# Optimization experiments

Measured on AMD Instinct MI355X. Metric: run time of the kernel, lower is better.

Reference implementation:

```python
import jax, jax.numpy as jnp
import numpy as np

B, T, C, H = 4, 2048, 1024, 16
D = C // H  # head_dim = 64

def setup_inputs() -> dict:
    key = jax.random.key(0)
    k1, k2, k3 = jax.random.split(key, 3)
    x = jax.random.normal(k1, (B, T, C), dtype=jnp.float32)
    W_attn = jax.random.normal(k2, (C, 3 * C), dtype=jnp.float32) * (C ** -0.5)
    b_attn = jnp.zeros((3 * C,), dtype=jnp.float32)
    W_proj = jax.random.normal(k3, (C, C), dtype=jnp.float32) * (C ** -0.5)
    b_proj = jnp.zeros((C,), dtype=jnp.float32)
    return {"x": x, "W_attn": W_attn, "b_attn": b_attn, "W_proj": W_proj, "b_proj": b_proj}

def reference(x, W_attn, b_attn, W_proj, b_proj):
    Bc, Tc, Cc = x.shape
    qkv = x @ W_attn + b_attn                       # [B,T,3C]
    q, k, v = jnp.split(qkv, 3, axis=-1)
    q = q.reshape(Bc, Tc, H, D).transpose(0, 2, 1, 3)  # [B,H,T,D]
    k = k.reshape(Bc, Tc, H, D).transpose(0, 2, 1, 3)
    v = v.reshape(Bc, Tc, H, D).transpose(0, 2, 1, 3)
    scores = jnp.einsum('bhqd,bhkd->bhqk', q, k) / jnp.sqrt(jnp.float32(D))
    causal = jnp.tril(jnp.ones((Tc, Tc), dtype=bool))
    scores = jnp.where(causal[None, None, :, :], scores, jnp.float32(-jnp.inf))
    wei = jax.nn.softmax(scores, axis=-1)           # dropout=0 -> identity
    out = jnp.einsum('bhqk,bhkd->bhqd', wei, v)     # [B,H,T,D]
    out = out.transpose(0, 2, 1, 3).reshape(Bc, Tc, Cc)
    return out @ W_proj + b_proj
```

## Files before the change

kernel.cpp:

```cpp
#include <hip/hip_runtime.h>
#include <cstdint>
#include <cstddef>

#define Bsz   4
#define Tsz   2048
#define Csz   1024
#define Hn    16
#define Dh    64
#define Mrows 8192
#define KD    1024

#define NEG_BIG (-1.0e30f)
#define SCL2  0.18033688011112042f

typedef unsigned short u16;
typedef __bf16  bf16x8 __attribute__((ext_vector_type(8)));
typedef __bf16  bf16x2 __attribute__((ext_vector_type(2)));
typedef float   f32x4  __attribute__((ext_vector_type(4)));
typedef unsigned int u32x4 __attribute__((ext_vector_type(4)));

#define BARRIER() do { asm volatile("" ::: "memory");                          \
                       __builtin_amdgcn_s_barrier();                           \
                       asm volatile("" ::: "memory"); } while (0)

__device__ __forceinline__ u16 f2bf(float f) {
  union { float f; unsigned int i; } v; v.f = f;
  unsigned int u = v.i;
  return (u16)((u + 0x7fffu + ((u >> 16) & 1u)) >> 16);
}
__device__ __forceinline__ unsigned int pack2bf(float a, float b) {
#if __has_builtin(__builtin_amdgcn_cvt_pk_bf16_f32)
  union { bf16x2 h; unsigned int u; } cv;
  cv.h = __builtin_amdgcn_cvt_pk_bf16_f32(a, b);
  return cv.u;
#else
  return (unsigned int)f2bf(a) | ((unsigned int)f2bf(b) << 16);
#endif
}
__device__ __forceinline__ unsigned int pack2bf_trunc(float lo, float hi) {
  return __builtin_amdgcn_perm(__builtin_bit_cast(unsigned int, hi),
                               __builtin_bit_cast(unsigned int, lo),
                               0x07060302u);
}
__device__ __forceinline__ float fast_exp2(float x) {
#if __has_builtin(__builtin_amdgcn_exp2f)
  return __builtin_amdgcn_exp2f(x);
#else
  return exp2f(x);
#endif
}

#define CVT_BLKS  (Mrows * Csz / 4 / 256)
#define TRA_BLKS  (48 * 16)
#define TRP_BLKS  (16 * 16)

__global__ __launch_bounds__(256)
void prep(const float* __restrict__ x, u16* __restrict__ xbf,
          const float* __restrict__ Wa, u16* __restrict__ WTa,
          const float* __restrict__ Wp, u16* __restrict__ WTp) {
  __shared__ u16 tile[64][65];
  int bid = blockIdx.x;
  const int tid = threadIdx.x;
  if (bid < CVT_BLKS) {
    const int i = bid * 256 + tid;
    const float4 v = ((const float4*)x)[i];
    uint2 o;
    o.x = pack2bf(v.x, v.y);
    o.y = pack2bf(v.z, v.w);
    ((uint2*)xbf)[i] = o;
    return;
  }
  bid -= CVT_BLKS;
  const float* in; u16* out; int cols, bx, by;
  if (bid < TRA_BLKS) {
    in = Wa; out = WTa; cols = 3 * Csz; bx = bid % 48; by = bid / 48;
  } else {
    bid -= TRA_BLKS;
    in = Wp; out = WTp; cols = Csz; bx = bid & 15; by = bid >> 4;
  }
  const int tc = bx * 64, tr = by * 64;
  const int xx = tid & 63, y0 = tid >> 6;
#pragma unroll
  for (int yy = 0; yy < 64; yy += 4) {
    int r = yy + y0;
    tile[r][xx] = f2bf(in[(size_t)(tr + r) * cols + tc + xx]);
  }
  __syncthreads();
#pragma unroll
  for (int yy = 0; yy < 64; yy += 4) {
    int r = yy + y0;
    out[(size_t)(tc + r) * Csz + tr + xx] = tile[xx][r];
  }
}

template<int MODE>
__global__ __launch_bounds__(256, 4)
void gemm_bt(const u16* __restrict__ A, const u16* __restrict__ BT,
             const float* __restrict__ bias, u16* __restrict__ o0,
             u16* __restrict__ o1, u16* __restrict__ o2,
             float* __restrict__ fout, int N) {
  __shared__ u16 lsA[2][128 * 32];
  __shared__ u16 lsB[2][128 * 32];
  const int tid  = threadIdx.x;
  const int lane = tid & 63;
  const int wid  = tid >> 6;
  const int wm   = wid & 1, wn = wid >> 1;
  const int quad = lane >> 4, l15 = lane & 15;
  const int rswz = (l15 >> 1) & 3;

  int bx, by;
  {
    const int nwg  = gridDim.x * gridDim.y;
    const int orig = (int)blockIdx.y * gridDim.x + (int)blockIdx.x;
    const int cpx  = nwg >> 3;
    const int swz  = (orig & 7) * cpx + (orig >> 3);
    bx = swz % gridDim.x; by = swz / gridDim.x;
  }
  const int m0 = by * 128, n0 = bx * 128;

  f32x4 acc[4][4];
#pragma unroll
  for (int i = 0; i < 4; ++i)
#pragma unroll
    for (int j = 0; j < 4; ++j) acc[i][j] = (f32x4){0.f, 0.f, 0.f, 0.f};

  const int srow   = lane >> 2;
  const int schunk = (lane & 3) ^ ((lane >> 3) & 3);
  const u16* gA = A  + (size_t)(m0 + wid * 32 + srow) * KD + schunk * 8;
  const u16* gB = BT + (size_t)(n0 + wid * 32 + srow) * KD + schunk * 8;

  auto gstage = [&](int t, int bb) {
#if __has_builtin(__builtin_amdgcn_global_load_lds)
#pragma unroll
    for (int i = 0; i < 2; ++i)
      __builtin_amdgcn_global_load_lds(
          (const __attribute__((address_space(1))) void*)(gA + (size_t)i * 16 * KD + t * 32),
          (__attribute__((address_space(3))) void*)(&lsA[bb][(wid * 32 + i * 16) * 32]),
          16, 0, 0);
#pragma unroll
    for (int i = 0; i < 2; ++i)
      __builtin_amdgcn_global_load_lds(
          (const __attribute__((address_space(1))) void*)(gB + (size_t)i * 16 * KD + t * 32),
          (__attribute__((address_space(3))) void*)(&lsB[bb][(wid * 32 + i * 16) * 32]),
          16, 0, 0);
#else
#pragma unroll
    for (int cc = 0; cc < 2; ++cc) {
      const int c = tid + cc * 256;
      const int rr = c >> 2, off = c & 3;
      const int dc = (off ^ ((rr >> 1) & 3)) << 3;
      *(uint4*)&lsA[bb][rr * 32 + dc] =
          *(const uint4*)&A[(size_t)(m0 + rr) * KD + t * 32 + off * 8];
    }
#pragma unroll
    for (int cc = 0; cc < 2; ++cc) {
      const int c = tid + cc * 256;
      const int rr = c >> 2, off = c & 3;
      const int dc = (off ^ ((rr >> 1) & 3)) << 3;
      *(uint4*)&lsB[bb][rr * 32 + dc] =
          *(const uint4*)&BT[(size_t)(n0 + rr) * KD + t * 32 + off * 8];
    }
#endif
  };

#define READ_B(n_) (*(const bf16x8*)                                           \
    &lsB[cur][(wn * 64 + (n_) * 16 + l15) * 32 + ((quad ^ rswz) << 3)])
#define READ_A(m_) (*(const bf16x8*)                                           \
    &lsA[cur][(wm * 64 + (m_) * 16 + l15) * 32 + ((quad ^ rswz) << 3)])
#define MFMA_ROW(m_, src)                                                      \
  __builtin_amdgcn_s_setprio(1);                                               \
  _Pragma("unroll")                                                            \
  for (int n = 0; n < 4; ++n)                                                  \
    acc[m_][n] = __builtin_amdgcn_mfma_f32_16x16x32_bf16(                      \
        src, bfv[n], acc[m_][n], 0, 0, 0);                                     \
  __builtin_amdgcn_s_setprio(0);

  gstage(0, 0);
  const int KT = KD / 32;
  for (int t = 0; t < KT; ++t) {
    const int cur = t & 1;
    if (t < KT - 1) {
      gstage(t + 1, cur ^ 1);
      asm volatile("s_waitcnt vmcnt(4)" ::: "memory");
    } else {
      asm volatile("s_waitcnt vmcnt(0)" ::: "memory");
    }
    BARRIER();

    bf16x8 bfv[4];
#pragma unroll
    for (int n = 0; n < 4; ++n) bfv[n] = READ_B(n);
    bf16x8 afA = READ_A(0);
    bf16x8 afB = READ_A(1);
    MFMA_ROW(0, afA);
    afA = READ_A(2);
    MFMA_ROW(1, afB);
    afB = READ_A(3);
    MFMA_ROW(2, afA);
    MFMA_ROW(3, afB);

    BARRIER();
  }
#undef READ_B
#undef READ_A
#undef MFMA_ROW

#pragma unroll
  for (int i = 0; i < 4; ++i) {
#pragma unroll
    for (int j = 0; j < 4; ++j) {
      const int colb = n0 + wn * 64 + j * 16 + l15;
      const float bv = bias[colb];
      float vals[4];
#pragma unroll
      for (int r = 0; r < 4; ++r) vals[r] = acc[i][j][r] + bv;
      const int row0 = m0 + wm * 64 + i * 16 + quad * 4;
      if (MODE == 0) {
        const int b = row0 >> 11, t0 = row0 & (Tsz - 1);
        const int region = colb >> 10;
        const int nc = colb & (Csz - 1);
        const int h = nc >> 6, d = nc & 63;
        if (region == 2) {
          uint2 st;
          st.x = pack2bf(vals[0], vals[1]);
          st.y = pack2bf(vals[2], vals[3]);
          *(uint2*)&o2[((size_t)((b << 4) + h) * Dh + d) * Tsz + t0] = st;
        } else {
          u16* dst = (region == 0) ? o0 : o1;
          const float qs = (region == 0) ? SCL2 : 1.0f;
#pragma unroll
          for (int r = 0; r < 4; ++r)
            dst[(size_t)(((b << 4) + h) * Tsz + t0 + r) * Dh + d] =
                f2bf(vals[r] * qs);
        }
      } else {
#pragma unroll
        for (int r = 0; r < 4; ++r)
          fout[(size_t)(row0 + r) * N + colb] = vals[r];
      }
    }
  }
}

__global__ __launch_bounds__(256)
void attn_fused(const u16* __restrict__ qb, const u16* __restrict__ kbuf,
                const u16* __restrict__ vT, u16* __restrict__ outp) {
  __shared__ u16 Kl[2][64 * 64];
  __shared__ u16 Vt[2][64 * 64];
  const int tid = threadIdx.x, lane = tid & 63, w = tid >> 6;
  const int quad = lane >> 4, l15 = lane & 15;
  const int cswz = (l15 & 7) << 3;
  const int bh = blockIdx.x;
  const int b = bh >> 4, h = bh & 15;
  const u16* Q   = qb   + (size_t)bh * Tsz * Dh;
  const u16* Kg  = kbuf + (size_t)bh * Tsz * Dh;
  const u16* VTg = vT   + (size_t)bh * Dh * Tsz;

  const int srow   = lane >> 3;
  const int schunk = ((lane & 7) ^ srow) << 3;
  const u16* gK0 = Kg  + (size_t)(w * 16 + srow) * Dh  + schunk;
  const u16* gV0 = VTg + (size_t)(w * 16 + srow) * Tsz + schunk;

#if __has_builtin(__builtin_amdgcn_global_load_lds)
#define STAGE(jj, bb) do {                                                     \
    const size_t kb_ = (size_t)(jj) * 64;                                      \
    _Pragma("unroll")                                                          \
    for (int i_ = 0; i_ < 2; ++i_) {                                           \
      __builtin_amdgcn_global_load_lds(                                        \
        (const __attribute__((address_space(1))) void*)(gK0 + (kb_ + (size_t)i_ * 8) * Dh), \
        (__attribute__((address_space(3))) void*)(&Kl[bb][(w * 16 + i_ * 8) * 64]), 16, 0, 0); \
      __builtin_amdgcn_global_load_lds(                                        \
        (const __attribute__((address_space(1))) void*)(gV0 + (size_t)(i_ * 8) * Tsz + kb_), \
        (__attribute__((address_space(3))) void*)(&Vt[bb][(w * 16 + i_ * 8) * 64]), 16, 0, 0); \
    }                                                                          \
  } while (0)
#else
#define STAGE(jj, bb) do {                                                     \
    const int kb_ = (jj) * 64;                                                 \
    _Pragma("unroll")                                                          \
    for (int cc_ = 0; cc_ < 2; ++cc_) {                                        \
      const int c_ = tid + cc_ * 256;                                          \
      const int rr_ = c_ >> 3, off_ = c_ & 7;                                  \
      const int dc_ = (off_ ^ (rr_ & 7)) << 3;                                 \
      *(uint4*)&Kl[bb][rr_ * 64 + dc_] =                                       \
          *(const uint4*)&Kg[(size_t)(kb_ + rr_) * Dh + off_ * 8];             \
      *(uint4*)&Vt[bb][rr_ * 64 + dc_] =                                       \
          *(const uint4*)&VTg[(size_t)rr_ * Tsz + kb_ + off_ * 8];             \
    }                                                                          \
  } while (0)
#endif

  for (int ph = 0; ph < 2; ++ph) {
    const int jq = ph ? (int)blockIdx.y : 31 - (int)blockIdx.y;

    const int qrow = jq * 64 + w * 16 + l15;
    const bf16x8 bq0 = *(const bf16x8*)&Q[(size_t)qrow * Dh + quad * 8];
    const bf16x8 bq1 = *(const bf16x8*)&Q[(size_t)qrow * Dh + 32 + quad * 8];

    f32x4 O[4];
#pragma unroll
    for (int nb = 0; nb < 4; ++nb) O[nb] = (f32x4){0.f, 0.f, 0.f, 0.f};
    float l_i = 0.f;

    STAGE(0, 0);

    for (int j = 0; j <= jq; ++j) {
      const int cur = j & 1;
      if (j < jq) {
        STAGE(j + 1, cur ^ 1);
        asm volatile("s_waitcnt vmcnt(4)" ::: "memory");
      } else {
        asm volatile("s_waitcnt vmcnt(0)" ::: "memory");
      }
      BARRIER();

      const int kb = j * 64;
      const bool diag = (j == jq);
      const int tmax = diag ? (w + 1) : 4;
      const u16* KT = Kl[cur];
      const u16* VL = Vt[cur];

      f32x4 S[4];
#pragma unroll
      for (int t = 0; t < 4; ++t) S[t] = (f32x4){0.f, 0.f, 0.f, 0.f};
      __builtin_amdgcn_s_setprio(1);
#pragma unroll
      for (int t = 0; t < 4; ++t) {
        if (t < tmax) {
          bf16x8 ak = *(const bf16x8*)&KT[(t * 16 + l15) * 64 + ((quad * 8) ^ cswz)];
          S[t] = __builtin_amdgcn_mfma_f32_16x16x32_bf16(ak, bq0, S[t], 0, 0, 0);
          ak = *(const bf16x8*)&KT[(t * 16 + l15) * 64 + ((quad * 8 + 32) ^ cswz)];
          S[t] = __builtin_amdgcn_mfma_f32_16x16x32_bf16(ak, bq1, S[t], 0, 0, 0);
        }
      }
      __builtin_amdgcn_s_setprio(0);

      float p[4][4];
      if (diag) {
#pragma unroll
        for (int t = 0; t < 4; ++t) {
          const int key0 = kb + t * 16 + quad * 4;
#pragma unroll
          for (int r = 0; r < 4; ++r) {
            const float sv =
                (t < tmax && key0 + r <= qrow) ? S[t][r] : NEG_BIG;
            p[t][r] = fast_exp2(sv);
            l_i += p[t][r];
          }
        }
      } else {
#pragma unroll
        for (int t = 0; t < 4; ++t)
#pragma unroll
          for (int r = 0; r < 4; ++r) {
            p[t][r] = fast_exp2(S[t][r]);
            l_i += p[t][r];
          }
      }

      u32x4 pu;
      pu[0] = pack2bf_trunc(p[0][0], p[0][1]);
      pu[1] = pack2bf_trunc(p[0][2], p[0][3]);
      pu[2] = pack2bf_trunc(p[1][0], p[1][1]);
      pu[3] = pack2bf_trunc(p[1][2], p[1][3]);
      bf16x8 pb = __builtin_bit_cast(bf16x8, pu);
      __builtin_amdgcn_s_setprio(1);
#pragma unroll
      for (int nb = 0; nb < 4; ++nb) {
        const uint2 a0 = *(const uint2*)&VL[(nb * 16 + l15) * 64 + ((quad * 4) ^ cswz)];
        const uint2 a1 = *(const uint2*)&VL[(nb * 16 + l15) * 64 + ((quad * 4 + 16) ^ cswz)];
        const u32x4 au = {a0.x, a0.y, a1.x, a1.y};
        O[nb] = __builtin_amdgcn_mfma_f32_16x16x32_bf16(
            __builtin_bit_cast(bf16x8, au), pb, O[nb], 0, 0, 0);
      }
      __builtin_amdgcn_s_setprio(0);
      if (tmax > 2) {
        pu[0] = pack2bf_trunc(p[2][0], p[2][1]);
        pu[1] = pack2bf_trunc(p[2][2], p[2][3]);
        pu[2] = pack2bf_trunc(p[3][0], p[3][1]);
        pu[3] = pack2bf_trunc(p[3][2], p[3][3]);
        pb = __builtin_bit_cast(bf16x8, pu);
        __builtin_amdgcn_s_setprio(1);
#pragma unroll
        for (int nb = 0; nb < 4; ++nb) {
          const uint2 a0 = *(const uint2*)&VL[(nb * 16 + l15) * 64 + ((quad * 4 + 32) ^ cswz)];
          const uint2 a1 = *(const uint2*)&VL[(nb * 16 + l15) * 64 + ((quad * 4 + 48) ^ cswz)];
          const u32x4 au = {a0.x, a0.y, a1.x, a1.y};
          O[nb] = __builtin_amdgcn_mfma_f32_16x16x32_bf16(
              __builtin_bit_cast(bf16x8, au), pb, O[nb], 0, 0, 0);
        }
        __builtin_amdgcn_s_setprio(0);
      }
      BARRIER();
    }

    float lt = l_i + __shfl_xor(l_i, 16, 64);
    lt += __shfl_xor(lt, 32, 64);
    const float inv = 1.0f / lt;
#pragma unroll
    for (int nb = 0; nb < 4; ++nb) {
      uint2 st;
      st.x = pack2bf(O[nb][0] * inv, O[nb][1] * inv);
      st.y = pack2bf(O[nb][2] * inv, O[nb][3] * inv);
      *(uint2*)&outp[(size_t)(b * Tsz + qrow) * Csz + h * Dh + nb * 16 + quad * 4] = st;
    }
  }
#undef STAGE
}

extern "C" void kernel_launch(void* const* d_in, const int* in_sizes, int n_in,
                              void* d_out, int out_size, void* d_ws, size_t ws_size,
                              hipStream_t stream) {
  const float* x      = (const float*)d_in[0];
  const float* W_attn = (const float*)d_in[1];
  const float* b_attn = (const float*)d_in[2];
  const float* W_proj = (const float*)d_in[3];
  const float* b_proj = (const float*)d_in[4];
  float* out = (float*)d_out;

  u16* ws   = (u16*)d_ws;
  u16* xbf  = ws;
  u16* qbuf = xbf  + (size_t)Mrows * Csz;
  u16* kbuf = qbuf + (size_t)Mrows * Csz;
  u16* vbuf = kbuf + (size_t)Mrows * Csz;
  u16* aout = vbuf + (size_t)Mrows * Csz;
  u16* WTa  = aout + (size_t)Mrows * Csz;
  u16* WTp  = WTa  + (size_t)Csz * 3 * Csz;

  prep<<<CVT_BLKS + TRA_BLKS + TRP_BLKS, 256, 0, stream>>>(
      x, xbf, W_attn, WTa, W_proj, WTp);
  gemm_bt<0><<<dim3(3 * Csz / 128, Mrows / 128), dim3(256), 0, stream>>>(
      xbf, WTa, b_attn, qbuf, kbuf, vbuf, nullptr, 3 * Csz);
  attn_fused<<<dim3(Bsz * Hn, Tsz / 128), 256, 0, stream>>>(
      qbuf, kbuf, vbuf, aout);
  gemm_bt<1><<<dim3(Csz / 128, Mrows / 128), dim3(256), 0, stream>>>(
      aout, WTp, b_proj, nullptr, nullptr, nullptr, out, Csz);
}
```

Baseline: 244.0 us.

## Templatize GEMM tiles, use 256-wide blocks with 4-stage LDS pipeline

The bf16 GEMM kernel is templated on block and warp tile sizes, and both projection GEMMs now launch 512-thread blocks with larger tiles (256x256 for QKV, 256x128 for output). The LDS ring grows from double to quad buffering, prefetching three k-steps ahead with matching vmcnt waits. The aim is more operand reuse per global load and deeper latency hiding. The cost is much more LDS and register use per block, fewer blocks, and possibly worse wave quantization on 256 CUs.

```diff
diff --git a/kernel.cpp b/kernel.cpp
--- a/kernel.cpp
+++ b/kernel.cpp
@@ -22,6 +22,16 @@
 #define BARRIER() do { asm volatile("" ::: "memory");                          \
                        __builtin_amdgcn_s_barrier();                           \
                        asm volatile("" ::: "memory"); } while (0)
+
+template<int N> __device__ __forceinline__ void vmwait() {
+  if constexpr (N >= 12)     asm volatile("s_waitcnt vmcnt(12)" ::: "memory");
+  else if constexpr (N == 9) asm volatile("s_waitcnt vmcnt(9)"  ::: "memory");
+  else if constexpr (N == 8) asm volatile("s_waitcnt vmcnt(8)"  ::: "memory");
+  else if constexpr (N == 6) asm volatile("s_waitcnt vmcnt(6)"  ::: "memory");
+  else if constexpr (N == 4) asm volatile("s_waitcnt vmcnt(4)"  ::: "memory");
+  else if constexpr (N == 3) asm volatile("s_waitcnt vmcnt(3)"  ::: "memory");
+  else                       asm volatile("s_waitcnt vmcnt(0)"  ::: "memory");
+}
 
 __device__ __forceinline__ u16 f2bf(float f) {
   union { float f; unsigned int i; } v; v.f = f;
@@ -93,18 +103,26 @@
   }
 }
 
-template<int MODE>
-__global__ __launch_bounds__(256, 4)
+template<int BM, int BN, int WM, int WN, int MODE>
+__global__ __launch_bounds__((BM / WM) * (BN / WN) * 64, 2)
 void gemm_bt(const u16* __restrict__ A, const u16* __restrict__ BT,
              const float* __restrict__ bias, u16* __restrict__ o0,
              u16* __restrict__ o1, u16* __restrict__ o2,
              float* __restrict__ fout, int N) {
-  __shared__ u16 lsA[2][128 * 32];
-  __shared__ u16 lsB[2][128 * 32];
+  constexpr int NW   = (BM / WM) * (BN / WN);
+  constexpr int WNV  = BN / WN;
+  constexpr int MF_M = WM / 16;
+  constexpr int MF_N = WN / 16;
+  constexpr int AI   = (BM / NW) / 16;
+  constexpr int BI   = (BN / NW) / 16;
+  constexpr int PI   = AI + BI;
+
+  __shared__ u16 lsA[4][BM * 32];
+  __shared__ u16 lsB[4][BN * 32];
   const int tid  = threadIdx.x;
   const int lane = tid & 63;
   const int wid  = tid >> 6;
-  const int wm   = wid & 1, wn = wid >> 1;
+  const int wm   = wid / WNV, wn = wid % WNV;
   const int quad = lane >> 4, l15 = lane & 15;
   const int rswz = (l15 >> 1) & 3;
 
@@ -116,45 +134,45 @@
     const int swz  = (orig & 7) * cpx + (orig >> 3);
     bx = swz % gridDim.x; by = swz / gridDim.x;
   }
-  const int m0 = by * 128, n0 = bx * 128;
-
-  f32x4 acc[4][4];
-#pragma unroll
-  for (int i = 0; i < 4; ++i)
-#pragma unroll
-    for (int j = 0; j < 4; ++j) acc[i][j] = (f32x4){0.f, 0.f, 0.f, 0.f};
+  const int m0 = by * BM, n0 = bx * BN;
+
+  f32x4 acc[MF_M][MF_N];
+#pragma unroll
+  for (int i = 0; i < MF_M; ++i)
+#pragma unroll
+    for (int j = 0; j < MF_N; ++j) acc[i][j] = (f32x4){0.f, 0.f, 0.f, 0.f};
 
   const int srow   = lane >> 2;
   const int schunk = (lane & 3) ^ ((lane >> 3) & 3);
-  const u16* gA = A  + (size_t)(m0 + wid * 32 + srow) * KD + schunk * 8;
-  const u16* gB = BT + (size_t)(n0 + wid * 32 + srow) * KD + schunk * 8;
+  const u16* gA = A  + (size_t)(m0 + wid * (BM / NW) + srow) * KD + schunk * 8;
+  const u16* gB = BT + (size_t)(n0 + wid * (BN / NW) + srow) * KD + schunk * 8;
 
   auto gstage = [&](int t, int bb) {
 #if __has_builtin(__builtin_amdgcn_global_load_lds)
 #pragma unroll
-    for (int i = 0; i < 2; ++i)
+    for (int i = 0; i < AI; ++i)
       __builtin_amdgcn_global_load_lds(
           (const __attribute__((address_space(1))) void*)(gA + (size_t)i * 16 * KD + t * 32),
-          (__attribute__((address_space(3))) void*)(&lsA[bb][(wid * 32 + i * 16) * 32]),
+          (__attribute__((address_space(3))) void*)(&lsA[bb][(wid * (BM / NW) + i * 16) * 32]),
           16, 0, 0);
 #pragma unroll
-    for (int i = 0; i < 2; ++i)
+    for (int i = 0; i < BI; ++i)
       __builtin_amdgcn_global_load_lds(
           (const __attribute__((address_space(1))) void*)(gB + (size_t)i * 16 * KD + t * 32),
-          (__attribute__((address_space(3))) void*)(&lsB[bb][(wid * 32 + i * 16) * 32]),
+          (__attribute__((address_space(3))) void*)(&lsB[bb][(wid * (BN / NW) + i * 16) * 32]),
           16, 0, 0);
 #else
 #pragma unroll
-    for (int cc = 0; cc < 2; ++cc) {
-      const int c = tid + cc * 256;
+    for (int cc = 0; cc < BM * 4 / (NW * 64); ++cc) {
+      const int c = tid + cc * NW * 64;
       const int rr = c >> 2, off = c & 3;
       const int dc = (off ^ ((rr >> 1) & 3)) << 3;
       *(uint4*)&lsA[bb][rr * 32 + dc] =
           *(const uint4*)&A[(size_t)(m0 + rr) * KD + t * 32 + off * 8];
     }
 #pragma unroll
-    for (int cc = 0; cc < 2; ++cc) {
-      const int c = tid + cc * 256;
+    for (int cc = 0; cc < BN * 4 / (NW * 64); ++cc) {
+      const int c = tid + cc * NW * 64;
       const int rr = c >> 2, off = c & 3;
       const int dc = (off ^ ((rr >> 1) & 3)) << 3;
       *(uint4*)&lsB[bb][rr * 32 + dc] =
@@ -164,57 +182,56 @@
   };
 
 #define READ_B(n_) (*(const bf16x8*)                                           \
-    &lsB[cur][(wn * 64 + (n_) * 16 + l15) * 32 + ((quad ^ rswz) << 3)])
+    &lsB[cur][(wn * WN + (n_) * 16 + l15) * 32 + ((quad ^ rswz) << 3)])
 #define READ_A(m_) (*(const bf16x8*)                                           \
-    &lsA[cur][(wm * 64 + (m_) * 16 + l15) * 32 + ((quad ^ rswz) << 3)])
-#define MFMA_ROW(m_, src)                                                      \
-  __builtin_amdgcn_s_setprio(1);                                               \
-  _Pragma("unroll")                                                            \
-  for (int n = 0; n < 4; ++n)                                                  \
-    acc[m_][n] = __builtin_amdgcn_mfma_f32_16x16x32_bf16(                      \
-        src, bfv[n], acc[m_][n], 0, 0, 0);                                     \
-  __builtin_amdgcn_s_setprio(0);
-
-  gstage(0, 0);
+    &lsA[cur][(wm * WM + (m_) * 16 + l15) * 32 + ((quad ^ rswz) << 3)])
+
+  gstage(0, 0); gstage(1, 1); gstage(2, 2);
   const int KT = KD / 32;
   for (int t = 0; t < KT; ++t) {
-    const int cur = t & 1;
-    if (t < KT - 1) {
-      gstage(t + 1, cur ^ 1);
-      asm volatile("s_waitcnt vmcnt(4)" ::: "memory");
-    } else {
-      asm volatile("s_waitcnt vmcnt(0)" ::: "memory");
-    }
+    const int cur = t & 3;
+    if (t + 3 < KT) {
+      gstage(t + 3, (t + 3) & 3);
+      vmwait<3 * PI>();
+    } else if (t == KT - 3) vmwait<2 * PI>();
+    else if (t == KT - 2)   vmwait<PI>();
+    else                    vmwait<0>();
     BARRIER();
 
-    bf16x8 bfv[4];
-#pragma unroll
-    for (int n = 0; n < 4; ++n) bfv[n] = READ_B(n);
-    bf16x8 afA = READ_A(0);
-    bf16x8 afB = READ_A(1);
-    MFMA_ROW(0, afA);
-    afA = READ_A(2);
-    MFMA_ROW(1, afB);
-    afB = READ_A(3);
-    MFMA_ROW(2, afA);
-    MFMA_ROW(3, afB);
+    bf16x8 bfv[MF_N];
+#pragma unroll
+    for (int n = 0; n < MF_N; ++n) bfv[n] = READ_B(n);
+    bf16x8 ar0 = READ_A(0);
+    bf16x8 ar1 = READ_A(1);
+#pragma unroll
+    for (int m = 0; m < MF_M; ++m) {
+      const bf16x8 am = (m & 1) ? ar1 : ar0;
+      if (m + 2 < MF_M) {
+        if (m & 1) ar1 = READ_A(m + 2); else ar0 = READ_A(m + 2);
+      }
+      __builtin_amdgcn_s_setprio(1);
+#pragma unroll
+      for (int n = 0; n < MF_N; ++n)
+        acc[m][n] = __builtin_amdgcn_mfma_f32_16x16x32_bf16(
+            am, bfv[n], acc[m][n], 0, 0, 0);
+      __builtin_amdgcn_s_setprio(0);
+    }
 
     BARRIER();
   }
 #undef READ_B
 #undef READ_A
-#undef MFMA_ROW
-
-#pragma unroll
-  for (int i = 0; i < 4; ++i) {
-#pragma unroll
-    for (int j = 0; j < 4; ++j) {
-      const int colb = n0 + wn * 64 + j * 16 + l15;
+
+#pragma unroll
+  for (int i = 0; i < MF_M; ++i) {
+#pragma unroll
+    for (int j = 0; j < MF_N; ++j) {
+      const int colb = n0 + wn * WN + j * 16 + l15;
       const float bv = bias[colb];
       float vals[4];
 #pragma unroll
       for (int r = 0; r < 4; ++r) vals[r] = acc[i][j][r] + bv;
-      const int row0 = m0 + wm * 64 + i * 16 + quad * 4;
+      const int row0 = m0 + wm * WM + i * 16 + quad * 4;
       if (MODE == 0) {
         const int b = row0 >> 11, t0 = row0 & (Tsz - 1);
         const int region = colb >> 10;
@@ -429,10 +446,12 @@
 
   prep<<<CVT_BLKS + TRA_BLKS + TRP_BLKS, 256, 0, stream>>>(
       x, xbf, W_attn, WTa, W_proj, WTp);
-  gemm_bt<0><<<dim3(3 * Csz / 128, Mrows / 128), dim3(256), 0, stream>>>(
+  gemm_bt<256, 256, 128, 64, 0><<<dim3(3 * Csz / 256, Mrows / 256),
+                                  dim3(512), 0, stream>>>(
       xbf, WTa, b_attn, qbuf, kbuf, vbuf, nullptr, 3 * Csz);
   attn_fused<<<dim3(Bsz * Hn, Tsz / 128), 256, 0, stream>>>(
       qbuf, kbuf, vbuf, aout);
-  gemm_bt<1><<<dim3(Csz / 128, Mrows / 128), dim3(256), 0, stream>>>(
+  gemm_bt<256, 128, 64, 64, 1><<<dim3(Csz / 128, Mrows / 256),
+                                 dim3(512), 0, stream>>>(
       aout, WTp, b_proj, nullptr, nullptr, nullptr, out, Csz);
 }
```

New measurement: 269.6 us. 1.1x slower.

## Template GEMM tile sizes with wider QKV tile; compute softmax row sums via MFMA

Applied to the files above, without the earlier changes.

The GEMM kernel becomes a template over block tile dimensions. The QKV projection now runs with 128x256 tiles and 8 waves per block, which gives more B-operand reuse per A load and cuts the grid to half as many blocks. In the attention kernel, the per-lane scalar accumulation of softmax probabilities and the closing cross-lane shuffle reduction are replaced by an extra MFMA against a ones vector, so the row sums come out of the matrix unit. The extra MFMA per step adds matrix-core work, and the larger GEMM block increases LDS and register pressure, which may lower occupancy.

```diff
diff --git a/kernel.cpp b/kernel.cpp
--- a/kernel.cpp
+++ b/kernel.cpp
@@ -22,6 +22,14 @@
 #define BARRIER() do { asm volatile("" ::: "memory");                          \
                        __builtin_amdgcn_s_barrier();                           \
                        asm volatile("" ::: "memory"); } while (0)
+
+template<int N> __device__ __forceinline__ void vmwait() {
+  if constexpr (N >= 8)      asm volatile("s_waitcnt vmcnt(8)"  ::: "memory");
+  else if constexpr (N == 6) asm volatile("s_waitcnt vmcnt(6)"  ::: "memory");
+  else if constexpr (N == 4) asm volatile("s_waitcnt vmcnt(4)"  ::: "memory");
+  else if constexpr (N == 3) asm volatile("s_waitcnt vmcnt(3)"  ::: "memory");
+  else                       asm volatile("s_waitcnt vmcnt(0)"  ::: "memory");
+}
 
 __device__ __forceinline__ u16 f2bf(float f) {
   union { float f; unsigned int i; } v; v.f = f;
@@ -93,18 +101,24 @@
   }
 }
 
-template<int MODE>
-__global__ __launch_bounds__(256, 4)
+template<int BM, int BN, int MODE>
+__global__ __launch_bounds__((BM / 64) * (BN / 64) * 64, 4)
 void gemm_bt(const u16* __restrict__ A, const u16* __restrict__ BT,
              const float* __restrict__ bias, u16* __restrict__ o0,
              u16* __restrict__ o1, u16* __restrict__ o2,
              float* __restrict__ fout, int N) {
-  __shared__ u16 lsA[2][128 * 32];
-  __shared__ u16 lsB[2][128 * 32];
+  constexpr int NW  = (BM / 64) * (BN / 64);
+  constexpr int WNV = BN / 64;
+  constexpr int AI  = (BM / NW) / 16;
+  constexpr int BI  = (BN / NW) / 16;
+  constexpr int PI  = AI + BI;
+
+  __shared__ u16 lsA[2][BM * 32];
+  __shared__ u16 lsB[2][BN * 32];
   const int tid  = threadIdx.x;
   const int lane = tid & 63;
   const int wid  = tid >> 6;
-  const int wm   = wid & 1, wn = wid >> 1;
+  const int wm   = wid / WNV, wn = wid % WNV;
   const int quad = lane >> 4, l15 = lane & 15;
   const int rswz = (l15 >> 1) & 3;
 
@@ -116,7 +130,7 @@
     const int swz  = (orig & 7) * cpx + (orig >> 3);
     bx = swz % gridDim.x; by = swz / gridDim.x;
   }
-  const int m0 = by * 128, n0 = bx * 128;
+  const int m0 = by * BM, n0 = bx * BN;
 
   f32x4 acc[4][4];
 #pragma unroll
@@ -126,35 +140,35 @@
 
   const int srow   = lane >> 2;
   const int schunk = (lane & 3) ^ ((lane >> 3) & 3);
-  const u16* gA = A  + (size_t)(m0 + wid * 32 + srow) * KD + schunk * 8;
-  const u16* gB = BT + (size_t)(n0 + wid * 32 + srow) * KD + schunk * 8;
+  const u16* gA = A  + (size_t)(m0 + wid * (BM / NW) + srow) * KD + schunk * 8;
+  const u16* gB = BT + (size_t)(n0 + wid * (BN / NW) + srow) * KD + schunk * 8;
 
   auto gstage = [&](int t, int bb) {
 #if __has_builtin(__builtin_amdgcn_global_load_lds)
 #pragma unroll
-    for (int i = 0; i < 2; ++i)
+    for (int i = 0; i < AI; ++i)
       __builtin_amdgcn_global_load_lds(
           (const __attribute__((address_space(1))) void*)(gA + (size_t)i * 16 * KD + t * 32),
-          (__attribute__((address_space(3))) void*)(&lsA[bb][(wid * 32 + i * 16) * 32]),
+          (__attribute__((address_space(3))) void*)(&lsA[bb][(wid * (BM / NW) + i * 16) * 32]),
           16, 0, 0);
 #pragma unroll
-    for (int i = 0; i < 2; ++i)
+    for (int i = 0; i < BI; ++i)
       __builtin_amdgcn_global_load_lds(
           (const __attribute__((address_space(1))) void*)(gB + (size_t)i * 16 * KD + t * 32),
-          (__attribute__((address_space(3))) void*)(&lsB[bb][(wid * 32 + i * 16) * 32]),
+          (__attribute__((address_space(3))) void*)(&lsB[bb][(wid * (BN / NW) + i * 16) * 32]),
           16, 0, 0);
 #else
 #pragma unroll
-    for (int cc = 0; cc < 2; ++cc) {
-      const int c = tid + cc * 256;
+    for (int cc = 0; cc < BM * 4 / (NW * 64); ++cc) {
+      const int c = tid + cc * NW * 64;
       const int rr = c >> 2, off = c & 3;
       const int dc = (off ^ ((rr >> 1) & 3)) << 3;
       *(uint4*)&lsA[bb][rr * 32 + dc] =
           *(const uint4*)&A[(size_t)(m0 + rr) * KD + t * 32 + off * 8];
     }
 #pragma unroll
-    for (int cc = 0; cc < 2; ++cc) {
-      const int c = tid + cc * 256;
+    for (int cc = 0; cc < BN * 4 / (NW * 64); ++cc) {
+      const int c = tid + cc * NW * 64;
       const int rr = c >> 2, off = c & 3;
       const int dc = (off ^ ((rr >> 1) & 3)) << 3;
       *(uint4*)&lsB[bb][rr * 32 + dc] =
@@ -181,9 +195,9 @@
     const int cur = t & 1;
     if (t < KT - 1) {
       gstage(t + 1, cur ^ 1);
-      asm volatile("s_waitcnt vmcnt(4)" ::: "memory");
+      vmwait<PI>();
     } else {
-      asm volatile("s_waitcnt vmcnt(0)" ::: "memory");
+      vmwait<0>();
     }
     BARRIER();
 
@@ -255,6 +269,9 @@
   const u16* Q   = qb   + (size_t)bh * Tsz * Dh;
   const u16* Kg  = kbuf + (size_t)bh * Tsz * Dh;
   const u16* VTg = vT   + (size_t)bh * Dh * Tsz;
+
+  const u32x4 onesu = {0x3F803F80u, 0x3F803F80u, 0x3F803F80u, 0x3F803F80u};
+  const bf16x8 ones = __builtin_bit_cast(bf16x8, onesu);
 
   const int srow   = lane >> 3;
   const int schunk = ((lane & 7) ^ srow) << 3;
@@ -300,7 +317,7 @@
     f32x4 O[4];
 #pragma unroll
     for (int nb = 0; nb < 4; ++nb) O[nb] = (f32x4){0.f, 0.f, 0.f, 0.f};
-    float l_i = 0.f;
+    f32x4 lmf = (f32x4){0.f, 0.f, 0.f, 0.f};
 
     STAGE(0, 0);
 
@@ -345,17 +362,14 @@
             const float sv =
                 (t < tmax && key0 + r <= qrow) ? S[t][r] : NEG_BIG;
             p[t][r] = fast_exp2(sv);
-            l_i += p[t][r];
           }
         }
       } else {
 #pragma unroll
         for (int t = 0; t < 4; ++t)
 #pragma unroll
-          for (int r = 0; r < 4; ++r) {
+          for (int r = 0; r < 4; ++r)
             p[t][r] = fast_exp2(S[t][r]);
-            l_i += p[t][r];
-          }
       }
 
       u32x4 pu;
@@ -373,6 +387,7 @@
         O[nb] = __builtin_amdgcn_mfma_f32_16x16x32_bf16(
             __builtin_bit_cast(bf16x8, au), pb, O[nb], 0, 0, 0);
       }
+      lmf = __builtin_amdgcn_mfma_f32_16x16x32_bf16(ones, pb, lmf, 0, 0, 0);
       __builtin_amdgcn_s_setprio(0);
       if (tmax > 2) {
         pu[0] = pack2bf_trunc(p[2][0], p[2][1]);
@@ -389,14 +404,13 @@
           O[nb] = __builtin_amdgcn_mfma_f32_16x16x32_bf16(
               __builtin_bit_cast(bf16x8, au), pb, O[nb], 0, 0, 0);
         }
+        lmf = __builtin_amdgcn_mfma_f32_16x16x32_bf16(ones, pb, lmf, 0, 0, 0);
         __builtin_amdgcn_s_setprio(0);
       }
       BARRIER();
     }
 
-    float lt = l_i + __shfl_xor(l_i, 16, 64);
-    lt += __shfl_xor(lt, 32, 64);
-    const float inv = 1.0f / lt;
+    const float inv = 1.0f / lmf[0];
 #pragma unroll
     for (int nb = 0; nb < 4; ++nb) {
       uint2 st;
@@ -429,10 +443,10 @@
 
   prep<<<CVT_BLKS + TRA_BLKS + TRP_BLKS, 256, 0, stream>>>(
       x, xbf, W_attn, WTa, W_proj, WTp);
-  gemm_bt<0><<<dim3(3 * Csz / 128, Mrows / 128), dim3(256), 0, stream>>>(
+  gemm_bt<128, 256, 0><<<dim3(3 * Csz / 256, Mrows / 128), dim3(512), 0, stream>>>(
       xbf, WTa, b_attn, qbuf, kbuf, vbuf, nullptr, 3 * Csz);
   attn_fused<<<dim3(Bsz * Hn, Tsz / 128), 256, 0, stream>>>(
       qbuf, kbuf, vbuf, aout);
-  gemm_bt<1><<<dim3(Csz / 128, Mrows / 128), dim3(256), 0, stream>>>(
+  gemm_bt<128, 128, 1><<<dim3(Csz / 128, Mrows / 128), dim3(256), 0, stream>>>(
       aout, WTp, b_proj, nullptr, nullptr, nullptr, out, Csz);
 }
```

Result: no change. 248.7 us (+1.9%).
